# Performance work log

Hardware: AMD Instinct MI355X
Metric: run time of the kernel (lower is better)

Reference implementation:

```python
import jax, jax.numpy as jnp
import numpy as np


def setup_inputs() -> dict:
    key = jax.random.key(0)
    k1, k2 = jax.random.split(key)
    B, L, D = 8, 4096, 1024
    hidden_states = jax.random.normal(k1, (B, L, D), dtype=jnp.float32)
    token_mask = jax.random.bernoulli(k2, 0.5, (B, L))
    return {"hidden_states": hidden_states, "token_mask": token_mask}


def reference(hidden_states, token_mask):
    """Compact hidden states at masked positions, left-packed and zero-padded.

    Returns (chunked: (B, M, D), counts: (B,)) where M = max tokens per row.
    Vectorized: prefix-sum over the mask gives per-row scatter destinations;
    masked-out positions are routed to a scratch slot M that is sliced off.
    """
    B, L, D = hidden_states.shape
    counts = token_mask.sum(axis=1).astype(jnp.int32)  # (B,)
    M = int(jnp.max(counts))  # data-dependent pad width (eager, matches .item())
    if M == 0:
        return hidden_states[:, :0, :], counts
    # destination index within each row: 0..count-1 for kept tokens, M for dropped
    dest = jnp.where(token_mask, jnp.cumsum(token_mask, axis=1) - 1, M)  # (B, L)
    b_idx = jnp.arange(B)[:, None]  # (B, 1)
    out = jnp.zeros((B, M + 1, D), hidden_states.dtype)
    out = out.at[b_idx, dest].set(hidden_states)  # single fused scatter
    chunked = out[:, :M, :]  # drop scratch slot
    return chunked, counts
```

## Files before the change

### kernel.cpp

```cpp
#include <hip/hip_runtime.h>
#include <hip/hip_bf16.h>


__global__ __launch_bounds__(1024) void scan_kernel(
        const int* __restrict__ mask,
        int* __restrict__ src_idx,
        int* __restrict__ counts_ws,
        float* __restrict__ counts_out,
        int L, int M) {
    const int b = blockIdx.x;
    const int t = threadIdx.x;
    const int lane = t & 63;
    const int wid  = t >> 6;
    const int base = t * 4;

    const int4 v = *(const int4*)(mask + (size_t)b * L + base);
    const int m0 = (v.x != 0), m1 = (v.y != 0), m2 = (v.z != 0), m3 = (v.w != 0);
    const int s = m0 + m1 + m2 + m3;

    int incl = s;
    #pragma unroll
    for (int off = 1; off < 64; off <<= 1) {
        int up = __shfl_up(incl, off, 64);
        if (lane >= off) incl += up;
    }

    __shared__ int wsum[16];
    __shared__ int wexc[17];
    if (lane == 63) wsum[wid] = incl;
    __syncthreads();
    if (t == 0) {
        int acc = 0;
        #pragma unroll
        for (int w = 0; w < 16; ++w) { wexc[w] = acc; acc += wsum[w]; }
        wexc[16] = acc;
        counts_ws[b] = acc;
        counts_out[b] = (float)acc;
    }
    __syncthreads();

    int prefix = wexc[wid] + (incl - s);

    int* srow = src_idx + (size_t)b * M;
    if (m0) srow[prefix++] = base + 0;
    if (m1) srow[prefix++] = base + 1;
    if (m2) srow[prefix++] = base + 2;
    if (m3) srow[prefix]   = base + 3;
}

__global__ __launch_bounds__(256) void pack_kernel(
        const float4* __restrict__ hidden,
        const int* __restrict__ src_idx,
        const int* __restrict__ counts,
        float4* __restrict__ out,
        int L, int M, int D4, int nrows) {
    const int t = threadIdx.x;
    for (int r = blockIdx.x; r < nrows; r += gridDim.x) {
        const int b = r / M;
        const int m = r - b * M;
        const size_t orow = (size_t)r * D4;
        if (m < counts[b]) {
            const int l = src_idx[r];
            const size_t irow = ((size_t)b * L + l) * D4;
            for (int i = t; i < D4; i += blockDim.x)
                out[orow + i] = hidden[irow + i];
        } else {
            const float4 z = make_float4(0.f, 0.f, 0.f, 0.f);
            for (int i = t; i < D4; i += blockDim.x)
                out[orow + i] = z;
        }
    }
}

extern "C" void kernel_launch(void* const* d_in, const int* in_sizes, int n_in,
                              void* d_out, int out_size, void* d_ws, size_t ws_size,
                              hipStream_t stream) {
    const int B = 8;
    const int BL = in_sizes[1];
    const int D  = in_sizes[0] / BL;
    const int L  = BL / B;
    const int M  = (out_size - B) / (B * D);

    const float* hidden = (const float*)d_in[0];
    const int*   mask   = (const int*)d_in[1];
    float*       out    = (float*)d_out;

    int* counts_ws = (int*)d_ws;
    int* src_idx   = (int*)d_ws + 64;

    float* counts_out = out + (size_t)B * M * D;

    scan_kernel<<<B, 1024, 0, stream>>>(mask, src_idx, counts_ws, counts_out, L, M);

    if (M > 0) {
        const int nrows = B * M;
        int grid = nrows < 2048 ? nrows : 2048;
        pack_kernel<<<grid, 256, 0, stream>>>((const float4*)hidden, src_idx,
                                              counts_ws, (float4*)out, L, M,
                                              D / 4, nrows);
    }
}
```

Baseline: 204.1 us.

## Fuse mask scan into pack kernel with per-block ballot prefix and nontemporal copies

Drops the separate scan kernel and the src_idx workspace. Each pack block re-reads its batch row's mask, builds 64-bit ballot words and a prefix over them in shared memory, then finds each output row's source token by binary search plus bit selection. Row copies use nontemporal loads and stores. This removes a kernel launch and the dependency between two kernels, but every block redundantly scans a 4096-entry mask and pays a serial bit-clear loop per row.

```diff
diff --git a/kernel.cpp b/kernel.cpp
--- a/kernel.cpp
+++ b/kernel.cpp
@@ -1,81 +1,92 @@
 #include <hip/hip_runtime.h>
-#include <hip/hip_bf16.h>
 
 
-__global__ __launch_bounds__(1024) void scan_kernel(
-        const int* __restrict__ mask,
-        int* __restrict__ src_idx,
-        int* __restrict__ counts_ws,
-        float* __restrict__ counts_out,
-        int L, int M) {
-    const int b = blockIdx.x;
-    const int t = threadIdx.x;
+typedef float floatx4 __attribute__((ext_vector_type(4)));
+
+__global__ __launch_bounds__(256) void fused_pack(
+        const floatx4* __restrict__ hidden,
+        const int*     __restrict__ mask,
+        floatx4*       __restrict__ out,
+        float*         __restrict__ counts_out,
+        int L, int M, int D4, int nrows, int rpb) {
+    __shared__ unsigned long long words[64];
+    __shared__ int excl[65];
+
+    const int t    = threadIdx.x;
     const int lane = t & 63;
     const int wid  = t >> 6;
-    const int base = t * 4;
 
-    const int4 v = *(const int4*)(mask + (size_t)b * L + base);
-    const int m0 = (v.x != 0), m1 = (v.y != 0), m2 = (v.z != 0), m3 = (v.w != 0);
-    const int s = m0 + m1 + m2 + m3;
+    int r = blockIdx.x * rpb;
+    const int r1 = min(nrows, r + rpb);
+    if (r >= r1) return;
 
-    int incl = s;
-    #pragma unroll
-    for (int off = 1; off < 64; off <<= 1) {
-        int up = __shfl_up(incl, off, 64);
-        if (lane >= off) incl += up;
+    while (r < r1) {
+        const int b = r / M;
+        const int mstart = r - b * M;
+        const int mend   = min(r1 - b * M, M);
+
+        const int* mrow = mask + (size_t)b * L;
+        #pragma unroll
+        for (int i = 0; i < 16; ++i) {
+            const int k = wid * 16 + i;
+            const unsigned long long bal = __ballot(mrow[k * 64 + lane] != 0);
+            if (lane == 0) words[k] = bal;
+        }
+        __syncthreads();
+
+        if (wid == 0) {
+            const int pc = __popcll(words[lane]);
+            int incl = pc;
+            #pragma unroll
+            for (int off = 1; off < 64; off <<= 1) {
+                const int up = __shfl_up(incl, off, 64);
+                if (lane >= off) incl += up;
+            }
+            excl[lane] = incl - pc;
+            if (lane == 63) excl[64] = incl;
+        }
+        __syncthreads();
+
+        const int cnt = excl[64];
+        if (t == 0) counts_out[b] = (float)cnt;
+
+        for (int m = mstart; m < mend; ++m, ++r) {
+            const size_t orow = ((size_t)b * M + m) * D4;
+            if (m < cnt) {
+                int lo = 0, hi = 63;
+                #pragma unroll
+                for (int s = 0; s < 6; ++s) {
+                    const int mid = (lo + hi + 1) >> 1;
+                    if (excl[mid] <= m) lo = mid; else hi = mid - 1;
+                }
+                unsigned long long w = words[lo];
+                const int j = m - excl[lo];
+                for (int q = 0; q < j; ++q) w &= w - 1;
+                const int l = lo * 64 + __builtin_ctzll(w);
+
+                const size_t irow = ((size_t)b * L + l) * D4;
+                for (int i = t; i < D4; i += 256) {
+                    const floatx4 v = __builtin_nontemporal_load(&hidden[irow + i]);
+                    __builtin_nontemporal_store(v, &out[orow + i]);
+                }
+            } else {
+                const floatx4 z = (floatx4){0.f, 0.f, 0.f, 0.f};
+                for (int i = t; i < D4; i += 256)
+                    __builtin_nontemporal_store(z, &out[orow + i]);
+            }
+        }
+        __syncthreads();
     }
-
-    __shared__ int wsum[16];
-    __shared__ int wexc[17];
-    if (lane == 63) wsum[wid] = incl;
-    __syncthreads();
-    if (t == 0) {
-        int acc = 0;
-        #pragma unroll
-        for (int w = 0; w < 16; ++w) { wexc[w] = acc; acc += wsum[w]; }
-        wexc[16] = acc;
-        counts_ws[b] = acc;
-        counts_out[b] = (float)acc;
-    }
-    __syncthreads();
-
-    int prefix = wexc[wid] + (incl - s);
-
-    int* srow = src_idx + (size_t)b * M;
-    if (m0) srow[prefix++] = base + 0;
-    if (m1) srow[prefix++] = base + 1;
-    if (m2) srow[prefix++] = base + 2;
-    if (m3) srow[prefix]   = base + 3;
 }
 
-__global__ __launch_bounds__(256) void pack_kernel(
-        const float4* __restrict__ hidden,
-        const int* __restrict__ src_idx,
-        const int* __restrict__ counts,
-        float4* __restrict__ out,
-        int L, int M, int D4, int nrows) {
-    const int t = threadIdx.x;
-    for (int r = blockIdx.x; r < nrows; r += gridDim.x) {
-        const int b = r / M;
-        const int m = r - b * M;
-        const size_t orow = (size_t)r * D4;
-        if (m < counts[b]) {
-            const int l = src_idx[r];
-            const size_t irow = ((size_t)b * L + l) * D4;
-            for (int i = t; i < D4; i += blockDim.x)
-                out[orow + i] = hidden[irow + i];
-        } else {
-            const float4 z = make_float4(0.f, 0.f, 0.f, 0.f);
-            for (int i = t; i < D4; i += blockDim.x)
-                out[orow + i] = z;
-        }
-    }
+__global__ void zero_counts(float* counts_out, int B) {
+    if ((int)threadIdx.x < B) counts_out[threadIdx.x] = 0.f;
 }
 
 extern "C" void kernel_launch(void* const* d_in, const int* in_sizes, int n_in,
                               void* d_out, int out_size, void* d_ws, size_t ws_size,
                               hipStream_t stream) {
-    const int B = 8;
+    const int B  = 8;
     const int BL = in_sizes[1];
     const int D  = in_sizes[0] / BL;
     const int L  = BL / B;
@@ -84,19 +95,17 @@
     const float* hidden = (const float*)d_in[0];
     const int*   mask   = (const int*)d_in[1];
     float*       out    = (float*)d_out;
+    float* counts_out   = out + (size_t)B * M * D;
 
-    int* counts_ws = (int*)d_ws;
-    int* src_idx   = (int*)d_ws + 64;
+    if (M == 0) {
+        zero_counts<<<1, 64, 0, stream>>>(counts_out, B);
+        return;
+    }
 
-    float* counts_out = out + (size_t)B * M * D;
-
-    scan_kernel<<<B, 1024, 0, stream>>>(mask, src_idx, counts_ws, counts_out, L, M);
-
-    if (M > 0) {
-        const int nrows = B * M;
-        int grid = nrows < 2048 ? nrows : 2048;
-        pack_kernel<<<grid, 256, 0, stream>>>((const float4*)hidden, src_idx,
-                                              counts_ws, (float4*)out, L, M,
-                                              D / 4, nrows);
-    }
+    const int nrows = B * M;
+    const int rpb   = (nrows + 2047) / 2048;
+    const int grid  = (nrows + rpb - 1) / rpb;
+    fused_pack<<<grid, 256, 0, stream>>>((const floatx4*)hidden, mask,
+                                         (floatx4*)out, counts_out,
+                                         L, M, D / 4, nrows, rpb);
 }
```

Result: no change. 202.6 us (median of 2 runs) (-0.7%).
